# Kernel tuning notes

Measured on AMD Instinct MI355X. Metric: run time of the kernel, lower is better.

Reference implementation:

```python
import jax, jax.numpy as jnp
import numpy as np

NUM_DEVICES = 8  # ROUTING_ROWS


def setup_inputs() -> dict:
    key = jax.random.key(0)
    k1, k2, k3 = jax.random.split(key, 3)
    T, H, E, K = 8192, 4096, 64, 2
    input_tensor = jax.random.normal(k1, (T, H), dtype=jnp.float32)
    expert_indices = jax.random.randint(k2, (T, K), 0, E, dtype=jnp.int32)
    expert_mapping = jax.random.randint(k3, (E,), 0, NUM_DEVICES, dtype=jnp.int32)
    return {
        "input_tensor": input_tensor,
        "expert_indices": expert_indices,
        "expert_mapping": expert_mapping,
    }


def reference(input_tensor, expert_indices, expert_mapping):
    # all_to_all_dispatch: replicate each token onto every device that hosts
    # one of its selected experts. Output: [D, T, H].
    # token_devices[t, k] = device hosting expert expert_indices[t, k]
    token_devices = expert_mapping[expert_indices]            # [T, K] int
    # mask[d, t] = token t is routed to device d (via any of its top-k experts)
    device_ids = jnp.arange(NUM_DEVICES, dtype=token_devices.dtype)  # [D]
    mask = jnp.any(token_devices[None, :, :] == device_ids[:, None, None], axis=-1)  # [D, T]
    dispatched = mask[:, :, None].astype(input_tensor.dtype) * input_tensor[None, :, :]  # [D, T, H]
    return dispatched
```

## Files before the change

kernel.cpp:

```cpp
#include <hip/hip_runtime.h>


#define T_TOK 8192
#define H_DIM 4096
#define NUM_DEV 8

typedef float vfloat4 __attribute__((ext_vector_type(4)));

__global__ __launch_bounds__(256)
void a2a_dispatch_kernel(const float* __restrict__ input,
                         const int* __restrict__ expert_indices,
                         const int* __restrict__ expert_mapping,
                         float* __restrict__ out)
{
    const unsigned bid = blockIdx.x;
    const unsigned d   = bid >> 13;
    const unsigned t   = bid & (T_TOK - 1);

    const int e0   = expert_indices[2u * t];
    const int e1   = expert_indices[2u * t + 1];
    const int dev0 = expert_mapping[e0];
    const int dev1 = expert_mapping[e1];
    const bool hit = (dev0 == (int)d) || (dev1 == (int)d);

    const vfloat4* __restrict__ in_row =
        (const vfloat4*)(input + (size_t)t * H_DIM);
    vfloat4* __restrict__ out_row =
        (vfloat4*)(out + (size_t)bid * H_DIM);

    if (hit) {
#pragma unroll
        for (int k = 0; k < 4; ++k) {
            vfloat4 v = in_row[threadIdx.x + k * 256];
            __builtin_nontemporal_store(v, &out_row[threadIdx.x + k * 256]);
        }
    } else {
        const vfloat4 z = (vfloat4)(0.f);
#pragma unroll
        for (int k = 0; k < 4; ++k) {
            __builtin_nontemporal_store(z, &out_row[threadIdx.x + k * 256]);
        }
    }
}

extern "C" void kernel_launch(void* const* d_in, const int* in_sizes, int n_in,
                              void* d_out, int out_size, void* d_ws, size_t ws_size,
                              hipStream_t stream) {
    const float* input          = (const float*)d_in[0];
    const int*   expert_indices = (const int*)d_in[1];
    const int*   expert_mapping = (const int*)d_in[2];
    float*       out            = (float*)d_out;

    const int grid = NUM_DEV * T_TOK;
    a2a_dispatch_kernel<<<grid, 256, 0, stream>>>(input, expert_indices,
                                                  expert_mapping, out);
}
```

Baseline: 1.151 ms.

## Zero output with memset and scatter-copy only the routed token rows

The single kernel that wrote every [device, token] row, either copied or zeroed, is replaced by two steps. A hipMemsetAsync clears the whole output, then a kernel with one block per (token, top-k slot) copies the input row to its target device's slot, and the second slot skips the copy when both experts map to the same device. The aim is to move the bulk zero-fill onto the driver's memset path and limit the kernel to the few routed rows. In exchange, routed rows are written twice (zero then data), each input row is read up to twice, there is an extra launch, and the nontemporal store hints are dropped.

```diff
diff --git a/kernel.cpp b/kernel.cpp
--- a/kernel.cpp
+++ b/kernel.cpp
@@ -4,42 +4,35 @@
 #define T_TOK 8192
 #define H_DIM 4096
 #define NUM_DEV 8
+#define TOPK 2
 
 typedef float vfloat4 __attribute__((ext_vector_type(4)));
 
 __global__ __launch_bounds__(256)
-void a2a_dispatch_kernel(const float* __restrict__ input,
-                         const int* __restrict__ expert_indices,
-                         const int* __restrict__ expert_mapping,
-                         float* __restrict__ out)
+void a2a_copy_rows_kernel(const float* __restrict__ input,
+                          const int* __restrict__ expert_indices,
+                          const int* __restrict__ expert_mapping,
+                          float* __restrict__ out)
 {
     const unsigned bid = blockIdx.x;
-    const unsigned d   = bid >> 13;
-    const unsigned t   = bid & (T_TOK - 1);
+    const unsigned t   = bid >> 1;
+    const unsigned k   = bid & 1;
 
-    const int e0   = expert_indices[2u * t];
-    const int e1   = expert_indices[2u * t + 1];
-    const int dev0 = expert_mapping[e0];
-    const int dev1 = expert_mapping[e1];
-    const bool hit = (dev0 == (int)d) || (dev1 == (int)d);
+    const int e   = expert_indices[TOPK * t + k];
+    const int dev = expert_mapping[e];
+    if (k == 1) {
+        const int e0 = expert_indices[TOPK * t];
+        if (expert_mapping[e0] == dev) return;
+    }
 
     const vfloat4* __restrict__ in_row =
         (const vfloat4*)(input + (size_t)t * H_DIM);
     vfloat4* __restrict__ out_row =
-        (vfloat4*)(out + (size_t)bid * H_DIM);
+        (vfloat4*)(out + ((size_t)dev * T_TOK + (size_t)t) * H_DIM);
 
-    if (hit) {
 #pragma unroll
-        for (int k = 0; k < 4; ++k) {
-            vfloat4 v = in_row[threadIdx.x + k * 256];
-            __builtin_nontemporal_store(v, &out_row[threadIdx.x + k * 256]);
-        }
-    } else {
-        const vfloat4 z = (vfloat4)(0.f);
-#pragma unroll
-        for (int k = 0; k < 4; ++k) {
-            __builtin_nontemporal_store(z, &out_row[threadIdx.x + k * 256]);
-        }
+    for (int i = 0; i < 4; ++i) {
+        out_row[threadIdx.x + i * 256] = in_row[threadIdx.x + i * 256];
     }
 }
 
@@ -51,7 +44,10 @@
     const int*   expert_mapping = (const int*)d_in[2];
     float*       out            = (float*)d_out;
 
-    const int grid = NUM_DEV * T_TOK;
-    a2a_dispatch_kernel<<<grid, 256, 0, stream>>>(input, expert_indices,
-                                                  expert_mapping, out);
+    const size_t out_bytes = (size_t)NUM_DEV * T_TOK * H_DIM * sizeof(float);
+    hipMemsetAsync(out, 0, out_bytes, stream);
+
+    const int grid = T_TOK * TOPK;
+    a2a_copy_rows_kernel<<<grid, 256, 0, stream>>>(input, expert_indices,
+                                                   expert_mapping, out);
 }
```

After: 1.140 ms. No clear change (-1.0%).
